# Optimization experiments

Measured on AMD Instinct MI355X. Metric: run time of the kernel, lower is better.

Reference implementation:

```python
import math
import jax, jax.numpy as jnp
import numpy as np

B, S, E, H, DK, NW = 2048, 1, 1024, 128, 8, 8  # d_k == n_wires == 8, seq_len must be 1
DIM = 2 ** NW


def setup_inputs() -> dict:
    key = jax.random.key(0)
    ks = jax.random.split(key, 7)
    scale = 1.0 / math.sqrt(E)
    return {
        "x": jax.random.normal(ks[0], (B, S, E), jnp.float32),
        "wq": jax.random.normal(ks[1], (E, E), jnp.float32) * scale,
        "wk": jax.random.normal(ks[2], (E, E), jnp.float32) * scale,
        "wv": jax.random.normal(ks[3], (E, E), jnp.float32) * scale,
        "wc": jax.random.normal(ks[4], (E, E), jnp.float32) * scale,
        "bc": jax.random.normal(ks[5], (E,), jnp.float32) * 0.01,
        "rx_params": jax.random.normal(ks[6], (NW,), jnp.float32),  # trainable RX angles (shared q_layer)
    }


def _apply_rx(state, theta, wire):
    # state: (N, 2,...,2) [NW qubit axes]; theta: scalar or (N,)
    N = state.shape[0]
    theta = jnp.broadcast_to(theta, (N,))
    c = jnp.cos(theta * 0.5).astype(jnp.complex64)[:, None]
    s = (-1j * jnp.sin(theta * 0.5).astype(jnp.complex64))[:, None]
    st = jnp.moveaxis(state, wire + 1, 1).reshape(N, 2, -1)
    new = jnp.stack([c * st[:, 0] + s * st[:, 1],
                     s * st[:, 0] + c * st[:, 1]], axis=1)
    return jnp.moveaxis(new.reshape((N,) + (2,) * NW), 1, wire + 1)


def _apply_cnot(state, ctrl, tgt):
    st = jnp.moveaxis(state, (ctrl + 1, tgt + 1), (1, 2))
    st = jnp.stack([st[:, 0], jnp.flip(st[:, 1], axis=1)], axis=1)
    return jnp.moveaxis(st, (1, 2), (ctrl + 1, tgt + 1))


def _qlayer(angles, rx_params):
    # angles: (N, NW) per-sample RX encoder angles; rx_params: (NW,) shared trainable RX
    N = angles.shape[0]
    state = jnp.zeros((N,) + (2,) * NW, jnp.complex64)
    state = state.at[(slice(None),) + (0,) * NW].set(1.0 + 0j)  # |0...0>
    for w in range(NW):
        state = _apply_rx(state, angles[:, w], w)      # encoder RX(x_w)
    for w in range(NW):
        state = _apply_rx(state, rx_params[w], w)      # trainable RX
    for w in range(NW - 1):
        state = _apply_cnot(state, w, w + 1)           # CNOT chain
    state = _apply_cnot(state, NW - 1, 0)              # ring closure
    probs = jnp.abs(state.reshape(N, DIM)) ** 2
    bits = (jnp.arange(DIM)[:, None] >> jnp.arange(NW - 1, -1, -1)[None, :]) & 1  # wire 0 = MSB
    signs = (1.0 - 2.0 * bits).astype(jnp.float32)     # (DIM, NW)
    return probs @ signs                               # <Z_w> per wire, (N, NW)


def reference(x, wq, wk, wv, wc, bc, rx_params):
    q = jnp.einsum('bse,fe->bsf', x, wq).reshape(B, S, H, DK)
    k = jnp.einsum('bse,fe->bsf', x, wk).reshape(B, S, H, DK)
    v = jnp.einsum('bse,fe->bsf', x, wv).reshape(B, S, H, DK)
    scores = jnp.einsum('bqhd,bkhd->bhqk', q, k) / math.sqrt(DK)
    attn = jax.nn.softmax(scores, axis=-1)             # dropout is identity in eval
    out = jnp.einsum('bhqk,bkhd->bqhd', attn, v).reshape(B, S, E)
    # per-head quantum circuit (S==1, d_k==NW); batch all heads together
    angles = out.reshape(B * H, DK)
    qout = _qlayer(angles, rx_params).reshape(B, S, E)
    return jnp.einsum('bse,fe->bsf', qout, wc) + bc
```

## Files before the change

### kernel.cpp

```cpp
#include <hip/hip_runtime.h>
#include <hip/hip_bf16.h>
#include <math.h>


#define BB 2048
#define EN 1024

typedef short s16x8 __attribute__((ext_vector_type(8)));
typedef float f32x4 __attribute__((ext_vector_type(4)));

union Frag { s16x8 v; __hip_bfloat16 h[8]; };

__device__ inline s16x8 cvt_frag(f32x4 lo, f32x4 hi) {
    Frag u;
    #pragma unroll
    for (int j = 0; j < 4; ++j) {
        u.h[j]     = __float2bfloat16(lo[j]);
        u.h[4 + j] = __float2bfloat16(hi[j]);
    }
    return u.v;
}

__device__ inline void gll16(const __hip_bfloat16* g, __hip_bfloat16* l) {
    __builtin_amdgcn_global_load_lds(
        (const __attribute__((address_space(1))) void*)g,
        (__attribute__((address_space(3))) void*)l,
        16, 0, 0);
}

__global__ __launch_bounds__(256) void cvt3_kernel(
        const float* __restrict__ x, const float* __restrict__ wv,
        const float* __restrict__ wc,
        __hip_bfloat16* __restrict__ xb, __hip_bfloat16* __restrict__ wvb,
        __hip_bfloat16* __restrict__ wcb)
{
    const int g = blockIdx.x * 256 + threadIdx.x;
    const int NX = (BB * EN) / 8;
    const int NG = (EN * EN) / 8;
    const float* s; __hip_bfloat16* d; size_t off;
    if (g < NX)           { s = x;  d = xb;  off = (size_t)g * 8; }
    else if (g < NX + NG) { s = wv; d = wvb; off = (size_t)(g - NX) * 8; }
    else                  { s = wc; d = wcb; off = (size_t)(g - NX - NG) * 8; }
    f32x4 lo = *(const f32x4*)(s + off);
    f32x4 hi = *(const f32x4*)(s + off + 4);
    *(s16x8*)(d + off) = cvt_frag(lo, hi);
}

template <int EPI>
__global__ __launch_bounds__(512, 4) void gemm_kernel(
        const __hip_bfloat16* __restrict__ A,
        const __hip_bfloat16* __restrict__ W,
        const float* __restrict__ bias, const float* __restrict__ rx,
        void* __restrict__ Cv)
{
    __shared__ __align__(16) unsigned char smem[32768];
    __hip_bfloat16* lds = (__hip_bfloat16*)smem;

    const int tid  = threadIdx.x;
    const int wave = tid >> 6, lane = tid & 63;
    const int l15 = lane & 15, lq = lane >> 4;
    const int m0 = blockIdx.x * 64, n0 = blockIdx.y * 64;
    const int wmt = wave >> 1;
    const int wnt = wave & 1;

    const __hip_bfloat16* gsrc[2];
    int ldst[2];
    #pragma unroll
    for (int i = 0; i < 2; ++i) {
        const int t = wave * 2 + i;
        int row, lofs;
        const __hip_bfloat16* base;
        if (t < 8) { const int mt = t >> 1; row = m0 + mt * 16 + l15; base = A; lofs = t * 512; }
        else       { const int u = t - 8;   row = n0 + (u >> 1) * 16 + l15; base = W; lofs = 4096 + u * 512; }
        gsrc[i] = base + (size_t)row * EN + (t & 1) * 32 + lq * 8;
        ldst[i] = lofs;
    }

    f32x4 acc[2] = {};

    #pragma unroll
    for (int i = 0; i < 2; ++i) gll16(gsrc[i], &lds[ldst[i]]);
    __syncthreads();

    int p = 0;
    for (int k0 = 64; k0 <= EN; k0 += 64) {
        if (k0 < EN) {
            const int q = p ^ 1;
            #pragma unroll
            for (int i = 0; i < 2; ++i) gll16(gsrc[i] + k0, &lds[q * 8192 + ldst[i]]);
        }
        const __hip_bfloat16* Ab = &lds[p * 8192];
        const __hip_bfloat16* Bb = Ab + 4096;
        #pragma unroll
        for (int kt = 0; kt < 2; ++kt) {
            s16x8 a = *(const s16x8*)&Ab[(wmt * 2 + kt) * 512 + lane * 8];
            #pragma unroll
            for (int j = 0; j < 2; ++j) {
                s16x8 b = *(const s16x8*)&Bb[((wnt * 2 + j) * 2 + kt) * 512 + lane * 8];
                acc[j] = __builtin_amdgcn_mfma_f32_16x16x32_bf16(a, b, acc[j], 0, 0, 0);
            }
        }
        __syncthreads();
        p ^= 1;
    }

    if (EPI == 0) {
        float* sb = (float*)smem;
        #pragma unroll
        for (int j = 0; j < 2; ++j) {
            const int col = wnt * 32 + j * 16 + l15;
            #pragma unroll
            for (int r = 0; r < 4; ++r)
                sb[(wmt * 16 + lq * 4 + r) * 68 + col] = acc[j][r];
        }
        __syncthreads();
        const int row = tid >> 3, g = tid & 7;
        const float* pv = &sb[row * 68 + g * 8];
        float t[8];
        #pragma unroll
        for (int j = 0; j < 8; ++j) t[j] = __cosf(pv[j] + rx[j]);
        Frag o;
        float suf = t[1];
        #pragma unroll
        for (int j = 2; j < 8; ++j) suf *= t[j];
        o.h[0] = __float2bfloat16(suf);
        float pr = t[0];
        #pragma unroll
        for (int j = 1; j < 8; ++j) { pr *= t[j]; o.h[j] = __float2bfloat16(pr); }
        __hip_bfloat16* V = (__hip_bfloat16*)Cv;
        *(s16x8*)(V + (size_t)(m0 + row) * EN + n0 + g * 8) = o.v;
    } else {
        float* C = (float*)Cv;
        #pragma unroll
        for (int j = 0; j < 2; ++j) {
            const int col = n0 + wnt * 32 + j * 16 + l15;
            const float bv = bias[col];
            #pragma unroll
            for (int r = 0; r < 4; ++r) {
                const int row = m0 + wmt * 16 + lq * 4 + r;
                C[(size_t)row * EN + col] = acc[j][r] + bv;
            }
        }
    }
}

extern "C" void kernel_launch(void* const* d_in, const int* in_sizes, int n_in,
                              void* d_out, int out_size, void* d_ws, size_t ws_size,
                              hipStream_t stream)
{
    const float* x  = (const float*)d_in[0];
    const float* wv = (const float*)d_in[3];
    const float* wc = (const float*)d_in[4];
    const float* bc = (const float*)d_in[5];
    const float* rx = (const float*)d_in[6];
    float* out = (float*)d_out;

    const size_t XE = (size_t)BB * EN;
    const size_t WE = (size_t)EN * EN;

    __hip_bfloat16* xb  = (__hip_bfloat16*)d_ws;
    __hip_bfloat16* wvb = xb + XE;
    __hip_bfloat16* wcb = wvb + WE;
    __hip_bfloat16* V   = wcb + WE;

    dim3 grid(BB / 64, EN / 64);
    cvt3_kernel<<<(int)((XE / 8 + 2 * (WE / 8)) / 256), 256, 0, stream>>>(
        x, wv, wc, xb, wvb, wcb);
    gemm_kernel<0><<<grid, 512, 0, stream>>>(xb, wvb, nullptr, rx, V);
    gemm_kernel<1><<<grid, 512, 0, stream>>>(V, wcb, bc, nullptr, out);
}
```

Before: 112.3 us.

## Fuse fp32-to-bf16 conversion into first GEMM and widen K-step to 128

Drops the separate conversion kernel. The first GEMM now loads fp32 x and wv straight from global memory, converts them in registers and writes bf16 into LDS, with software prefetch into registers. The same kernel also converts a slice of wc for the second GEMM. Both GEMMs now step K by 128 with a larger 64KB LDS double buffer. This removes the bf16 copies of x and wv plus one kernel launch, but the first GEMM now reads fp32 global data twice per tile use, and the larger LDS may cut occupancy.

After: 121.4 us. +8.1%, slower.

```diff
diff --git a/kernel.cpp b/kernel.cpp
--- a/kernel.cpp
+++ b/kernel.cpp
@@ -28,33 +28,12 @@
         16, 0, 0);
 }
 
-__global__ __launch_bounds__(256) void cvt3_kernel(
+__global__ __launch_bounds__(512, 4) void gemm1q_kernel(
         const float* __restrict__ x, const float* __restrict__ wv,
-        const float* __restrict__ wc,
-        __hip_bfloat16* __restrict__ xb, __hip_bfloat16* __restrict__ wvb,
-        __hip_bfloat16* __restrict__ wcb)
+        const float* __restrict__ wc, const float* __restrict__ rx,
+        __hip_bfloat16* __restrict__ wcb, __hip_bfloat16* __restrict__ V)
 {
-    const int g = blockIdx.x * 256 + threadIdx.x;
-    const int NX = (BB * EN) / 8;
-    const int NG = (EN * EN) / 8;
-    const float* s; __hip_bfloat16* d; size_t off;
-    if (g < NX)           { s = x;  d = xb;  off = (size_t)g * 8; }
-    else if (g < NX + NG) { s = wv; d = wvb; off = (size_t)(g - NX) * 8; }
-    else                  { s = wc; d = wcb; off = (size_t)(g - NX - NG) * 8; }
-    f32x4 lo = *(const f32x4*)(s + off);
-    f32x4 hi = *(const f32x4*)(s + off + 4);
-    *(s16x8*)(d + off) = cvt_frag(lo, hi);
-}
-
-template <int EPI>
-__global__ __launch_bounds__(512, 4) void gemm_kernel(
-        const __hip_bfloat16* __restrict__ A,
-        const __hip_bfloat16* __restrict__ W,
-        const float* __restrict__ bias, const float* __restrict__ rx,
-        void* __restrict__ Cv)
-{
-    __shared__ __align__(16) unsigned char smem[32768];
-    __hip_bfloat16* lds = (__hip_bfloat16*)smem;
+    __shared__ __align__(16) __hip_bfloat16 lds[32768];
 
     const int tid  = threadIdx.x;
     const int wave = tid >> 6, lane = tid & 63;
@@ -62,84 +41,155 @@
     const int m0 = blockIdx.x * 64, n0 = blockIdx.y * 64;
     const int wmt = wave >> 1;
     const int wnt = wave & 1;
-
-    const __hip_bfloat16* gsrc[2];
-    int ldst[2];
-    #pragma unroll
-    for (int i = 0; i < 2; ++i) {
-        const int t = wave * 2 + i;
-        int row, lofs;
-        const __hip_bfloat16* base;
-        if (t < 8) { const int mt = t >> 1; row = m0 + mt * 16 + l15; base = A; lofs = t * 512; }
-        else       { const int u = t - 8;   row = n0 + (u >> 1) * 16 + l15; base = W; lofs = 4096 + u * 512; }
-        gsrc[i] = base + (size_t)row * EN + (t & 1) * 32 + lq * 8;
-        ldst[i] = lofs;
+    const int bid = blockIdx.x + 32 * blockIdx.y;
+
+    if (tid < 256) {
+        const size_t off = (size_t)bid * 2048 + tid * 8;
+        f32x4 lo = *(const f32x4*)(wc + off);
+        f32x4 hi = *(const f32x4*)(wc + off + 4);
+        *(s16x8*)(wcb + off) = cvt_frag(lo, hi);
+    }
+
+    const float* gsrc[4];
+    int ldst[4];
+    #pragma unroll
+    for (int i = 0; i < 4; ++i) {
+        const int t = wave * 4 + i;
+        const int kt = t & 3;
+        const float* base;
+        int row;
+        if (t < 16) { base = x;  row = m0 + (t >> 2) * 16 + l15; }
+        else        { base = wv; row = n0 + ((t - 16) >> 2) * 16 + l15; }
+        gsrc[i] = base + (size_t)row * EN + kt * 32 + lq * 8;
+        ldst[i] = t * 512 + lane * 8;
     }
 
     f32x4 acc[2] = {};
-
-    #pragma unroll
-    for (int i = 0; i < 2; ++i) gll16(gsrc[i], &lds[ldst[i]]);
+    f32x4 lo[4], hi[4];
+
+    #pragma unroll
+    for (int i = 0; i < 4; ++i) { lo[i] = *(const f32x4*)gsrc[i]; hi[i] = *(const f32x4*)(gsrc[i] + 4); }
+    #pragma unroll
+    for (int i = 0; i < 4; ++i) *(s16x8*)&lds[ldst[i]] = cvt_frag(lo[i], hi[i]);
     __syncthreads();
 
     int p = 0;
-    for (int k0 = 64; k0 <= EN; k0 += 64) {
-        if (k0 < EN) {
-            const int q = p ^ 1;
-            #pragma unroll
-            for (int i = 0; i < 2; ++i) gll16(gsrc[i] + k0, &lds[q * 8192 + ldst[i]]);
-        }
-        const __hip_bfloat16* Ab = &lds[p * 8192];
-        const __hip_bfloat16* Bb = Ab + 4096;
-        #pragma unroll
-        for (int kt = 0; kt < 2; ++kt) {
-            s16x8 a = *(const s16x8*)&Ab[(wmt * 2 + kt) * 512 + lane * 8];
+    for (int it = 1; it <= 8; ++it) {
+        if (it < 8) {
+            #pragma unroll
+            for (int i = 0; i < 4; ++i) {
+                lo[i] = *(const f32x4*)(gsrc[i] + it * 128);
+                hi[i] = *(const f32x4*)(gsrc[i] + it * 128 + 4);
+            }
+        }
+        const __hip_bfloat16* Ab = &lds[p * 16384];
+        const __hip_bfloat16* Bb = Ab + 8192;
+        #pragma unroll
+        for (int kt = 0; kt < 4; ++kt) {
+            s16x8 a = *(const s16x8*)&Ab[(wmt * 4 + kt) * 512 + lane * 8];
             #pragma unroll
             for (int j = 0; j < 2; ++j) {
-                s16x8 b = *(const s16x8*)&Bb[((wnt * 2 + j) * 2 + kt) * 512 + lane * 8];
+                s16x8 b = *(const s16x8*)&Bb[((wnt * 2 + j) * 4 + kt) * 512 + lane * 8];
                 acc[j] = __builtin_amdgcn_mfma_f32_16x16x32_bf16(a, b, acc[j], 0, 0, 0);
             }
         }
+        if (it < 8) {
+            const int q = p ^ 1;
+            #pragma unroll
+            for (int i = 0; i < 4; ++i) *(s16x8*)&lds[q * 16384 + ldst[i]] = cvt_frag(lo[i], hi[i]);
+        }
         __syncthreads();
         p ^= 1;
     }
 
-    if (EPI == 0) {
-        float* sb = (float*)smem;
-        #pragma unroll
-        for (int j = 0; j < 2; ++j) {
-            const int col = wnt * 32 + j * 16 + l15;
-            #pragma unroll
-            for (int r = 0; r < 4; ++r)
-                sb[(wmt * 16 + lq * 4 + r) * 68 + col] = acc[j][r];
+    float* sb = (float*)lds;
+    #pragma unroll
+    for (int j = 0; j < 2; ++j) {
+        const int col = wnt * 32 + j * 16 + l15;
+        #pragma unroll
+        for (int r = 0; r < 4; ++r)
+            sb[(wmt * 16 + lq * 4 + r) * 68 + col] = acc[j][r];
+    }
+    __syncthreads();
+    const int row = tid >> 3, g = tid & 7;
+    const float* pv = &sb[row * 68 + g * 8];
+    float t[8];
+    #pragma unroll
+    for (int j = 0; j < 8; ++j) t[j] = __cosf(pv[j] + rx[j]);
+    Frag o;
+    float suf = t[1];
+    #pragma unroll
+    for (int j = 2; j < 8; ++j) suf *= t[j];
+    o.h[0] = __float2bfloat16(suf);
+    float pr = t[0];
+    #pragma unroll
+    for (int j = 1; j < 8; ++j) { pr *= t[j]; o.h[j] = __float2bfloat16(pr); }
+    *(s16x8*)(V + (size_t)(m0 + row) * EN + n0 + g * 8) = o.v;
+}
+
+__global__ __launch_bounds__(512, 4) void gemm2_kernel(
+        const __hip_bfloat16* __restrict__ V,
+        const __hip_bfloat16* __restrict__ wcb,
+        const float* __restrict__ bc, float* __restrict__ out)
+{
+    __shared__ __align__(16) __hip_bfloat16 lds[32768];
+
+    const int tid  = threadIdx.x;
+    const int wave = tid >> 6, lane = tid & 63;
+    const int l15 = lane & 15, lq = lane >> 4;
+    const int m0 = blockIdx.x * 64, n0 = blockIdx.y * 64;
+    const int wmt = wave >> 1, wnt = wave & 1;
+
+    const __hip_bfloat16* gsrc[4];
+    int ldst[4];
+    #pragma unroll
+    for (int i = 0; i < 4; ++i) {
+        const int t = wave * 4 + i;
+        const int kt = t & 3;
+        const __hip_bfloat16* base;
+        int row;
+        if (t < 16) { base = V;   row = m0 + (t >> 2) * 16 + l15; }
+        else        { base = wcb; row = n0 + ((t - 16) >> 2) * 16 + l15; }
+        gsrc[i] = base + (size_t)row * EN + kt * 32 + lq * 8;
+        ldst[i] = t * 512;
+    }
+
+    f32x4 acc[2] = {};
+
+    #pragma unroll
+    for (int i = 0; i < 4; ++i) gll16(gsrc[i], &lds[ldst[i]]);
+    __syncthreads();
+
+    int p = 0;
+    for (int it = 1; it <= 8; ++it) {
+        if (it < 8) {
+            const int q = p ^ 1;
+            #pragma unroll
+            for (int i = 0; i < 4; ++i) gll16(gsrc[i] + it * 128, &lds[q * 16384 + ldst[i]]);
+        }
+        const __hip_bfloat16* Ab = &lds[p * 16384];
+        const __hip_bfloat16* Bb = Ab + 8192;
+        #pragma unroll
+        for (int kt = 0; kt < 4; ++kt) {
+            s16x8 a = *(const s16x8*)&Ab[(wmt * 4 + kt) * 512 + lane * 8];
+            #pragma unroll
+            for (int j = 0; j < 2; ++j) {
+                s16x8 b = *(const s16x8*)&Bb[((wnt * 2 + j) * 4 + kt) * 512 + lane * 8];
+                acc[j] = __builtin_amdgcn_mfma_f32_16x16x32_bf16(a, b, acc[j], 0, 0, 0);
+            }
         }
         __syncthreads();
-        const int row = tid >> 3, g = tid & 7;
-        const float* pv = &sb[row * 68 + g * 8];
-        float t[8];
-        #pragma unroll
-        for (int j = 0; j < 8; ++j) t[j] = __cosf(pv[j] + rx[j]);
-        Frag o;
-        float suf = t[1];
-        #pragma unroll
-        for (int j = 2; j < 8; ++j) suf *= t[j];
-        o.h[0] = __float2bfloat16(suf);
-        float pr = t[0];
-        #pragma unroll
-        for (int j = 1; j < 8; ++j) { pr *= t[j]; o.h[j] = __float2bfloat16(pr); }
-        __hip_bfloat16* V = (__hip_bfloat16*)Cv;
-        *(s16x8*)(V + (size_t)(m0 + row) * EN + n0 + g * 8) = o.v;
-    } else {
-        float* C = (float*)Cv;
-        #pragma unroll
-        for (int j = 0; j < 2; ++j) {
-            const int col = n0 + wnt * 32 + j * 16 + l15;
-            const float bv = bias[col];
-            #pragma unroll
-            for (int r = 0; r < 4; ++r) {
-                const int row = m0 + wmt * 16 + lq * 4 + r;
-                C[(size_t)row * EN + col] = acc[j][r] + bv;
-            }
+        p ^= 1;
+    }
+
+    #pragma unroll
+    for (int j = 0; j < 2; ++j) {
+        const int col = n0 + wnt * 32 + j * 16 + l15;
+        const float bv = bc[col];
+        #pragma unroll
+        for (int r = 0; r < 4; ++r) {
+            const int row = m0 + wmt * 16 + lq * 4 + r;
+            out[(size_t)row * EN + col] = acc[j][r] + bv;
         }
     }
 }
@@ -155,17 +205,11 @@
     const float* rx = (const float*)d_in[6];
     float* out = (float*)d_out;
 
-    const size_t XE = (size_t)BB * EN;
     const size_t WE = (size_t)EN * EN;
-
-    __hip_bfloat16* xb  = (__hip_bfloat16*)d_ws;
-    __hip_bfloat16* wvb = xb + XE;
-    __hip_bfloat16* wcb = wvb + WE;
+    __hip_bfloat16* wcb = (__hip_bfloat16*)d_ws;
     __hip_bfloat16* V   = wcb + WE;
 
     dim3 grid(BB / 64, EN / 64);
-    cvt3_kernel<<<(int)((XE / 8 + 2 * (WE / 8)) / 256), 256, 0, stream>>>(
-        x, wv, wc, xb, wvb, wcb);
-    gemm_kernel<0><<<grid, 512, 0, stream>>>(xb, wvb, nullptr, rx, V);
-    gemm_kernel<1><<<grid, 512, 0, stream>>>(V, wcb, bc, nullptr, out);
-}
+    gemm1q_kernel<<<grid, 512, 0, stream>>>(x, wv, wc, rx, wcb, V);
+    gemm2_kernel<<<grid, 512, 0, stream>>>(V, wcb, bc, out);
+}
```

## Fuse both GEMMs into one cooperative kernel with per-row-block counters

Applied to the files above, without the earlier changes.

Merges the two GEMM launches into a single cooperative kernel of 512 blocks. Each block computes its tile of the first GEMM and quantum epilogue, then waits on an atomic counter until all 16 column tiles of its 64-row block are written before computing the second GEMM tile. This aims to remove one kernel launch and the full-grid barrier between the GEMMs. It adds spin-waiting and relies on all 512 blocks being co-resident, which the cooperative launch enforces.

Result: slower. 179.1 us (+59.5%).

```diff
diff --git a/kernel.cpp b/kernel.cpp
--- a/kernel.cpp
+++ b/kernel.cpp
@@ -32,9 +32,10 @@
         const float* __restrict__ x, const float* __restrict__ wv,
         const float* __restrict__ wc,
         __hip_bfloat16* __restrict__ xb, __hip_bfloat16* __restrict__ wvb,
-        __hip_bfloat16* __restrict__ wcb)
+        __hip_bfloat16* __restrict__ wcb, int* __restrict__ cnt)
 {
     const int g = blockIdx.x * 256 + threadIdx.x;
+    if (g < 32) cnt[g] = 0;
     const int NX = (BB * EN) / 8;
     const int NG = (EN * EN) / 8;
     const float* s; __hip_bfloat16* d; size_t off;
@@ -47,31 +48,26 @@
 }
 
 template <int EPI>
-__global__ __launch_bounds__(512, 4) void gemm_kernel(
+__device__ __forceinline__ void gemm_body(
         const __hip_bfloat16* __restrict__ A,
         const __hip_bfloat16* __restrict__ W,
         const float* __restrict__ bias, const float* __restrict__ rx,
-        void* __restrict__ Cv)
+        void* __restrict__ Cv, int m0, int n0, int tid,
+        __hip_bfloat16* lds)
 {
-    __shared__ __align__(16) unsigned char smem[32768];
-    __hip_bfloat16* lds = (__hip_bfloat16*)smem;
-
-    const int tid  = threadIdx.x;
     const int wave = tid >> 6, lane = tid & 63;
     const int l15 = lane & 15, lq = lane >> 4;
-    const int m0 = blockIdx.x * 64, n0 = blockIdx.y * 64;
-    const int wmt = wave >> 1;
-    const int wnt = wave & 1;
+    const int wmt = wave >> 1, wnt = wave & 1;
 
     const __hip_bfloat16* gsrc[2];
     int ldst[2];
     #pragma unroll
     for (int i = 0; i < 2; ++i) {
         const int t = wave * 2 + i;
+        const __hip_bfloat16* base;
         int row, lofs;
-        const __hip_bfloat16* base;
-        if (t < 8) { const int mt = t >> 1; row = m0 + mt * 16 + l15; base = A; lofs = t * 512; }
-        else       { const int u = t - 8;   row = n0 + (u >> 1) * 16 + l15; base = W; lofs = 4096 + u * 512; }
+        if (t < 8) { base = A; row = m0 + (t >> 1) * 16 + l15; lofs = t * 512; }
+        else       { const int u = t - 8; base = W; row = n0 + (u >> 1) * 16 + l15; lofs = 4096 + u * 512; }
         gsrc[i] = base + (size_t)row * EN + (t & 1) * 32 + lq * 8;
         ldst[i] = lofs;
     }
@@ -83,11 +79,11 @@
     __syncthreads();
 
     int p = 0;
-    for (int k0 = 64; k0 <= EN; k0 += 64) {
-        if (k0 < EN) {
+    for (int it = 1; it <= 16; ++it) {
+        if (it < 16) {
             const int q = p ^ 1;
             #pragma unroll
-            for (int i = 0; i < 2; ++i) gll16(gsrc[i] + k0, &lds[q * 8192 + ldst[i]]);
+            for (int i = 0; i < 2; ++i) gll16(gsrc[i] + it * 64, &lds[q * 8192 + ldst[i]]);
         }
         const __hip_bfloat16* Ab = &lds[p * 8192];
         const __hip_bfloat16* Bb = Ab + 4096;
@@ -105,7 +101,7 @@
     }
 
     if (EPI == 0) {
-        float* sb = (float*)smem;
+        float* sb = (float*)lds;
         #pragma unroll
         for (int j = 0; j < 2; ++j) {
             const int col = wnt * 32 + j * 16 + l15;
@@ -144,6 +140,35 @@
     }
 }
 
+__global__ __launch_bounds__(512, 4) void fused2_kernel(
+        const __hip_bfloat16* __restrict__ xb,
+        const __hip_bfloat16* __restrict__ wvb,
+        const __hip_bfloat16* __restrict__ wcb,
+        const float* __restrict__ bc, const float* __restrict__ rx,
+        __hip_bfloat16* __restrict__ V, int* __restrict__ cnt,
+        float* __restrict__ out)
+{
+    __shared__ __align__(16) __hip_bfloat16 lds[16384];
+    const int tid = threadIdx.x;
+    const int mi = blockIdx.x >> 4, ni = blockIdx.x & 15;
+    const int m0 = mi * 64, n0 = ni * 64;
+
+    gemm_body<0>(xb, wvb, nullptr, rx, V, m0, n0, tid, lds);
+    __syncthreads();
+
+    if (tid == 0) {
+        __threadfence();
+        __hip_atomic_fetch_add(&cnt[mi], 1, __ATOMIC_RELEASE,
+                               __HIP_MEMORY_SCOPE_AGENT);
+        while (__hip_atomic_load(&cnt[mi], __ATOMIC_ACQUIRE,
+                                 __HIP_MEMORY_SCOPE_AGENT) < 16)
+            __builtin_amdgcn_s_sleep(2);
+    }
+    __syncthreads();
+
+    gemm_body<1>(V, wcb, bc, nullptr, out, m0, n0, tid, lds);
+}
+
 extern "C" void kernel_launch(void* const* d_in, const int* in_sizes, int n_in,
                               void* d_out, int out_size, void* d_ws, size_t ws_size,
                               hipStream_t stream)
@@ -162,10 +187,13 @@
     __hip_bfloat16* wvb = xb + XE;
     __hip_bfloat16* wcb = wvb + WE;
     __hip_bfloat16* V   = wcb + WE;
+    int* cnt = (int*)(V + XE);
 
-    dim3 grid(BB / 64, EN / 64);
     cvt3_kernel<<<(int)((XE / 8 + 2 * (WE / 8)) / 256), 256, 0, stream>>>(
-        x, wv, wc, xb, wvb, wcb);
-    gemm_kernel<0><<<grid, 512, 0, stream>>>(xb, wvb, nullptr, rx, V);
-    gemm_kernel<1><<<grid, 512, 0, stream>>>(V, wcb, bc, nullptr, out);
+        x, wv, wc, xb, wvb, wcb, cnt);
+
+    void* args[] = { (void*)&xb, (void*)&wvb, (void*)&wcb, (void*)&bc,
+                     (void*)&rx, (void*)&V, (void*)&cnt, (void*)&out };
+    hipLaunchCooperativeKernel((const void*)fused2_kernel,
+                               dim3(512), dim3(512), args, 0, stream);
 }
```

## Use per-wave private LDS staging with vmcnt waits instead of block barriers

Applied to the files above, without the earlier changes.

Each block now runs 4 waves instead of 8, and each wave computes a 32x32 sub-tile. Each wave loads its own A and W slices into a private LDS region via global_load_lds and double-buffers them with s_waitcnt vmcnt, which removes the __syncthreads from the K loop. Every wave gets twice the MFMA work per loaded fragment, but A and W rows are now loaded redundantly across waves rather than shared through LDS, so global and L2 traffic goes up.

After: 140.2 us. +24.9%, slower.

```diff
diff --git a/kernel.cpp b/kernel.cpp
--- a/kernel.cpp
+++ b/kernel.cpp
@@ -47,99 +47,100 @@
 }
 
 template <int EPI>
-__global__ __launch_bounds__(512, 4) void gemm_kernel(
+__global__ __launch_bounds__(256, 4) void gemm_kernel(
         const __hip_bfloat16* __restrict__ A,
         const __hip_bfloat16* __restrict__ W,
         const float* __restrict__ bias, const float* __restrict__ rx,
         void* __restrict__ Cv)
 {
-    __shared__ __align__(16) unsigned char smem[32768];
-    __hip_bfloat16* lds = (__hip_bfloat16*)smem;
+    __shared__ __align__(16) __hip_bfloat16 lds[16384];
 
     const int tid  = threadIdx.x;
     const int wave = tid >> 6, lane = tid & 63;
     const int l15 = lane & 15, lq = lane >> 4;
     const int m0 = blockIdx.x * 64, n0 = blockIdx.y * 64;
-    const int wmt = wave >> 1;
-    const int wnt = wave & 1;
+    const int wm = (wave & 1) * 32, wn = (wave >> 1) * 32;
 
-    const __hip_bfloat16* gsrc[2];
-    int ldst[2];
-    #pragma unroll
-    for (int i = 0; i < 2; ++i) {
-        const int t = wave * 2 + i;
-        int row, lofs;
-        const __hip_bfloat16* base;
-        if (t < 8) { const int mt = t >> 1; row = m0 + mt * 16 + l15; base = A; lofs = t * 512; }
-        else       { const int u = t - 8;   row = n0 + (u >> 1) * 16 + l15; base = W; lofs = 4096 + u * 512; }
-        gsrc[i] = base + (size_t)row * EN + (t & 1) * 32 + lq * 8;
-        ldst[i] = lofs;
-    }
+    __hip_bfloat16* wbase = &lds[wave * 4096];
 
-    f32x4 acc[2] = {};
+    const __hip_bfloat16* gsrc[4];
+    gsrc[0] = A + (size_t)(m0 + wm +      l15) * EN + lq * 8;
+    gsrc[1] = A + (size_t)(m0 + wm + 16 + l15) * EN + lq * 8;
+    gsrc[2] = W + (size_t)(n0 + wn +      l15) * EN + lq * 8;
+    gsrc[3] = W + (size_t)(n0 + wn + 16 + l15) * EN + lq * 8;
+
+    f32x4 acc[2][2] = {};
 
     #pragma unroll
-    for (int i = 0; i < 2; ++i) gll16(gsrc[i], &lds[ldst[i]]);
-    __syncthreads();
+    for (int i = 0; i < 4; ++i) gll16(gsrc[i], wbase + i * 512);
 
     int p = 0;
-    for (int k0 = 64; k0 <= EN; k0 += 64) {
-        if (k0 < EN) {
-            const int q = p ^ 1;
+    for (int it = 1; it <= 32; ++it) {
+        if (it < 32) {
+            __hip_bfloat16* dst = wbase + (p ^ 1) * 2048;
             #pragma unroll
-            for (int i = 0; i < 2; ++i) gll16(gsrc[i] + k0, &lds[q * 8192 + ldst[i]]);
+            for (int i = 0; i < 4; ++i) gll16(gsrc[i] + it * 32, dst + i * 512);
+            asm volatile("s_waitcnt vmcnt(4)" ::: "memory");
+        } else {
+            asm volatile("s_waitcnt vmcnt(0)" ::: "memory");
         }
-        const __hip_bfloat16* Ab = &lds[p * 8192];
-        const __hip_bfloat16* Bb = Ab + 4096;
-        #pragma unroll
-        for (int kt = 0; kt < 2; ++kt) {
-            s16x8 a = *(const s16x8*)&Ab[(wmt * 2 + kt) * 512 + lane * 8];
-            #pragma unroll
-            for (int j = 0; j < 2; ++j) {
-                s16x8 b = *(const s16x8*)&Bb[((wnt * 2 + j) * 2 + kt) * 512 + lane * 8];
-                acc[j] = __builtin_amdgcn_mfma_f32_16x16x32_bf16(a, b, acc[j], 0, 0, 0);
-            }
-        }
-        __syncthreads();
+        const __hip_bfloat16* buf = wbase + p * 2048;
+        s16x8 a0 = *(const s16x8*)(buf +        lane * 8);
+        s16x8 a1 = *(const s16x8*)(buf +  512 + lane * 8);
+        s16x8 b0 = *(const s16x8*)(buf + 1024 + lane * 8);
+        s16x8 b1 = *(const s16x8*)(buf + 1536 + lane * 8);
+        acc[0][0] = __builtin_amdgcn_mfma_f32_16x16x32_bf16(a0, b0, acc[0][0], 0, 0, 0);
+        acc[0][1] = __builtin_amdgcn_mfma_f32_16x16x32_bf16(a0, b1, acc[0][1], 0, 0, 0);
+        acc[1][0] = __builtin_amdgcn_mfma_f32_16x16x32_bf16(a1, b0, acc[1][0], 0, 0, 0);
+        acc[1][1] = __builtin_amdgcn_mfma_f32_16x16x32_bf16(a1, b1, acc[1][1], 0, 0, 0);
         p ^= 1;
     }
 
     if (EPI == 0) {
-        float* sb = (float*)smem;
+        __syncthreads();
+        float* sb = (float*)lds;
         #pragma unroll
-        for (int j = 0; j < 2; ++j) {
-            const int col = wnt * 32 + j * 16 + l15;
+        for (int mi = 0; mi < 2; ++mi)
             #pragma unroll
-            for (int r = 0; r < 4; ++r)
-                sb[(wmt * 16 + lq * 4 + r) * 68 + col] = acc[j][r];
+            for (int nj = 0; nj < 2; ++nj) {
+                const int col = wn + nj * 16 + l15;
+                #pragma unroll
+                for (int r = 0; r < 4; ++r)
+                    sb[(wm + mi * 16 + lq * 4 + r) * 68 + col] = acc[mi][nj][r];
+            }
+        __syncthreads();
+        __hip_bfloat16* V = (__hip_bfloat16*)Cv;
+        #pragma unroll
+        for (int q = 0; q < 2; ++q) {
+            const int idx = q * 256 + tid;
+            const int row = idx >> 3, g = idx & 7;
+            const float* pv = &sb[row * 68 + g * 8];
+            float t[8];
+            #pragma unroll
+            for (int j = 0; j < 8; ++j) t[j] = __cosf(pv[j] + rx[j]);
+            Frag o;
+            float suf = t[1];
+            #pragma unroll
+            for (int j = 2; j < 8; ++j) suf *= t[j];
+            o.h[0] = __float2bfloat16(suf);
+            float pr = t[0];
+            #pragma unroll
+            for (int j = 1; j < 8; ++j) { pr *= t[j]; o.h[j] = __float2bfloat16(pr); }
+            *(s16x8*)(V + (size_t)(m0 + row) * EN + n0 + g * 8) = o.v;
         }
-        __syncthreads();
-        const int row = tid >> 3, g = tid & 7;
-        const float* pv = &sb[row * 68 + g * 8];
-        float t[8];
-        #pragma unroll
-        for (int j = 0; j < 8; ++j) t[j] = __cosf(pv[j] + rx[j]);
-        Frag o;
-        float suf = t[1];
-        #pragma unroll
-        for (int j = 2; j < 8; ++j) suf *= t[j];
-        o.h[0] = __float2bfloat16(suf);
-        float pr = t[0];
-        #pragma unroll
-        for (int j = 1; j < 8; ++j) { pr *= t[j]; o.h[j] = __float2bfloat16(pr); }
-        __hip_bfloat16* V = (__hip_bfloat16*)Cv;
-        *(s16x8*)(V + (size_t)(m0 + row) * EN + n0 + g * 8) = o.v;
     } else {
         float* C = (float*)Cv;
         #pragma unroll
-        for (int j = 0; j < 2; ++j) {
-            const int col = n0 + wnt * 32 + j * 16 + l15;
+        for (int nj = 0; nj < 2; ++nj) {
+            const int col = n0 + wn + nj * 16 + l15;
             const float bv = bias[col];
             #pragma unroll
-            for (int r = 0; r < 4; ++r) {
-                const int row = m0 + wmt * 16 + lq * 4 + r;
-                C[(size_t)row * EN + col] = acc[j][r] + bv;
-            }
+            for (int mi = 0; mi < 2; ++mi)
+                #pragma unroll
+                for (int r = 0; r < 4; ++r) {
+                    const int row = m0 + wm + mi * 16 + lq * 4 + r;
+                    C[(size_t)row * EN + col] = acc[mi][nj][r] + bv;
+                }
         }
     }
 }
@@ -166,6 +167,6 @@
     dim3 grid(BB / 64, EN / 64);
     cvt3_kernel<<<(int)((XE / 8 + 2 * (WE / 8)) / 256), 256, 0, stream>>>(
         x, wv, wc, xb, wvb, wcb);
-    gemm_kernel<0><<<grid, 512, 0, stream>>>(xb, wvb, nullptr, rx, V);
-    gemm_kernel<1><<<grid, 512, 0, stream>>>(V, wcb, bc, nullptr, out);
+    gemm_kernel<0><<<grid, 256, 0, stream>>>(xb, wvb, nullptr, rx, V);
+    gemm_kernel<1><<<grid, 256, 0, stream>>>(V, wcb, bc, nullptr, out);
 }
```
